# Kernel tuning notes

Measured on AMD Instinct MI355X. Metric: run time of the kernel, lower is better.

## Reference

```python
import jax, jax.numpy as jnp
import numpy as np

N_HEADS = 16


def layernorm(x, g, b, eps=1e-5):
    mu = jnp.mean(x, axis=-1, keepdims=True)
    var = jnp.var(x, axis=-1, keepdims=True)
    return (x - mu) * jax.lax.rsqrt(var + eps) * g + b


def mha(x, w_qkv, b_qkv, w_o, b_o, n_heads):
    # standard multi-head self-attention (dropout off / eval mode)
    B, S, D = x.shape
    hd = D // n_heads
    qkv = x @ w_qkv + b_qkv                      # [B,S,3D]
    q, k, v = jnp.split(qkv, 3, axis=-1)
    q = q.reshape(B, S, n_heads, hd).transpose(0, 2, 1, 3)  # bhsd
    k = k.reshape(B, S, n_heads, hd).transpose(0, 2, 1, 3)
    v = v.reshape(B, S, n_heads, hd).transpose(0, 2, 1, 3)
    att = jnp.einsum('bhqd,bhkd->bhqk', q, k) / jnp.sqrt(jnp.asarray(hd, x.dtype))
    att = jax.nn.softmax(att, axis=-1)
    out = jnp.einsum('bhqk,bhkd->bhqd', att, v)
    out = out.transpose(0, 2, 1, 3).reshape(B, S, D)
    return out @ w_o + b_o


def setup_inputs() -> dict:
    key = jax.random.key(0)
    ks = jax.random.split(key, 12)
    B, Sx, Sz, D = 4, 1024, 1024, 1024
    H = D * 4
    s = 0.02
    return {
        'x': jax.random.normal(ks[0], (B, Sx, D), jnp.float32),
        'z': jax.random.normal(ks[1], (B, Sz, D), jnp.float32),
        'g1': jnp.ones((D,), jnp.float32),
        'b1': jnp.zeros((D,), jnp.float32),
        'w_qkv': jax.random.normal(ks[2], (D, 3 * D), jnp.float32) * s,
        'b_qkv': jnp.zeros((3 * D,), jnp.float32),
        'w_o': jax.random.normal(ks[3], (D, D), jnp.float32) * s,
        'b_o': jnp.zeros((D,), jnp.float32),
        'w_kv': jax.random.normal(ks[4], (D, 2 * D), jnp.float32) * s,
        'b_kv': jnp.zeros((2 * D,), jnp.float32),
        'g2': jnp.ones((D,), jnp.float32),
        'b2': jnp.zeros((D,), jnp.float32),
        'w_m1': jax.random.normal(ks[5], (D, H), jnp.float32) * s,
        'b_m1': jnp.zeros((H,), jnp.float32),
        'w_m2': jax.random.normal(ks[6], (H, D), jnp.float32) * s,
        'b_m2': jnp.zeros((D,), jnp.float32),
    }


def reference(x, z, g1, b1, w_qkv, b_qkv, w_o, b_o, w_kv, b_kv, g2, b2, w_m1, b_m1, w_m2, b_m2):
    # q = x + self_mha(ln1(x))
    q = x + mha(layernorm(x, g1, b1), w_qkv, b_qkv, w_o, b_o, N_HEADS)
    # single-head cross attention: k,v from z, scale by sqrt(dim)
    kv = z @ w_kv + b_kv
    k, v = jnp.split(kv, 2, axis=-1)            # each [B,Sz,D]
    scale = jnp.sqrt(jnp.asarray(k.shape[-1], x.dtype))
    att = jax.nn.softmax(jnp.einsum('bqd,bkd->bqk', q, k) / scale, axis=-1)
    out = jnp.einsum('bqk,bkd->bqd', att, v)
    # out = out + mlp(ln2(out))
    h = layernorm(out, g2, b2)
    h = jax.nn.gelu(h @ w_m1 + b_m1) @ w_m2 + b_m2
    return out + h
```

## Files before the change

### kernel.cpp

```cpp
#include <hip/hip_runtime.h>
#include <cstdint>
#include <cstddef>

using u16 = unsigned short;

typedef __attribute__((ext_vector_type(4))) float f32x4;
typedef __attribute__((ext_vector_type(8))) short bf16x8;

#define DEV static __device__ __forceinline__

DEV float bf2f(u16 v) {
  union { unsigned u; float f; } x; x.u = ((unsigned)v) << 16; return x.f;
}
DEV u16 f2bf(float f) {
  union { float f; unsigned u; } x; x.f = f;
  unsigned r = x.u + 0x7fffu + ((x.u >> 16) & 1u);
  return (u16)(r >> 16);
}
DEV void gload16(const void* g, void* l) {
  __builtin_amdgcn_global_load_lds((const __attribute__((address_space(1))) void*)g,
                                   (__attribute__((address_space(3))) void*)l, 16, 0, 0);
}
DEV float fast_gelu(float x) {
  float y = 0.7978845608028654f * (x + 0.044715f * x * x * x);
  y = fminf(fmaxf(y, -15.0f), 15.0f);
  float e = __expf(2.0f * y);
  float t = (e - 1.0f) / (e + 1.0f);
  return 0.5f * x * (1.0f + t);
}

DEV float rowmax16_dpp(float v) {
  union { float f; int i; } a, b;
  a.f = v;
  b.i = __builtin_amdgcn_update_dpp(0, a.i, 0x121, 0xf, 0xf, true); a.f = fmaxf(a.f, b.f);
  b.i = __builtin_amdgcn_update_dpp(0, a.i, 0x122, 0xf, 0xf, true); a.f = fmaxf(a.f, b.f);
  b.i = __builtin_amdgcn_update_dpp(0, a.i, 0x124, 0xf, 0xf, true); a.f = fmaxf(a.f, b.f);
  b.i = __builtin_amdgcn_update_dpp(0, a.i, 0x128, 0xf, 0xf, true); a.f = fmaxf(a.f, b.f);
  return a.f;
}

template <typename OutT, bool GELU, int BN, bool SPLIT>
__global__ __launch_bounds__(256, 2) void gemm_nt(
    const u16* __restrict__ A, const u16* __restrict__ Bt, OutT* __restrict__ C,
    int K, int lda, int ldb, int ldc,
    const float* __restrict__ bias,
    const float* __restrict__ resF, const u16* __restrict__ resB, int ldr,
    float scale,
    long long sA, long long sB, long long sC, long long sR,
    int kSlices)
{
  constexpr int NW = (BN == 128) ? 64 : 32;
  constexpr int NJ = NW / 16;
  __shared__ u16 As[128 * 32];
  __shared__ u16 Bs[BN * 32];

  const int z = blockIdx.z;
  const int bz = z / kSlices;
  const int ks = z - bz * kSlices;
  const int Ksl = K / kSlices;
  const int kbeg = ks * Ksl, kend = kbeg + Ksl;

  A  += (size_t)bz * sA;
  Bt += (size_t)bz * sB;
  if constexpr (SPLIT) C += (size_t)ks * sC;
  else                 C += (size_t)bz * sC;
  const int m0 = blockIdx.y * 128, n0 = blockIdx.x * BN;
  const int tid = threadIdx.x;
  const int lane = tid & 63, wave = tid >> 6;
  const int wm = (wave >> 1) * 64, wn = (wave & 1) * NW;
  const int m15 = lane & 15, quad = lane >> 4;

  const u16* Ab = A + (size_t)m0 * lda;
  const u16* Bb = Bt + (size_t)n0 * ldb;
  const int r0 = tid >> 2, cc8 = (tid & 3) * 8;

  f32x4 acc[4][NJ];
#pragma unroll
  for (int i = 0; i < 4; i++)
#pragma unroll
    for (int j = 0; j < NJ; j++) acc[i][j] = (f32x4){0.f, 0.f, 0.f, 0.f};

  for (int k0 = kbeg; k0 < kend; k0 += 32) {
    __syncthreads();
    gload16(Ab + (size_t)r0 * lda + k0 + cc8,        &As[tid * 8]);
    gload16(Ab + (size_t)(r0 + 64) * lda + k0 + cc8, &As[2048 + tid * 8]);
    gload16(Bb + (size_t)r0 * ldb + k0 + cc8,        &Bs[tid * 8]);
    if constexpr (BN == 128)
      gload16(Bb + (size_t)(r0 + 64) * ldb + k0 + cc8, &Bs[2048 + tid * 8]);
    __syncthreads();
    bf16x8 af[4], bfr[NJ];
#pragma unroll
    for (int i = 0; i < 4; i++) af[i]  = *(const bf16x8*)&As[(wm + i * 16 + m15) * 32 + quad * 8];
#pragma unroll
    for (int j = 0; j < NJ; j++) bfr[j] = *(const bf16x8*)&Bs[(wn + j * 16 + m15) * 32 + quad * 8];
#pragma unroll
    for (int i = 0; i < 4; i++)
#pragma unroll
      for (int j = 0; j < NJ; j++)
        acc[i][j] = __builtin_amdgcn_mfma_f32_16x16x32_bf16(af[i], bfr[j], acc[i][j], 0, 0, 0);
  }

  const float* resFb = resF ? resF + (size_t)bz * sR : nullptr;
  const u16*   resBb = resB ? resB + (size_t)bz * sR : nullptr;

#pragma unroll
  for (int i = 0; i < 4; i++) {
    const int rowb = m0 + wm + i * 16 + quad * 4;
#pragma unroll
    for (int r = 0; r < 4; r++) {
      const size_t rowoff = (size_t)(rowb + r) * ldc;
      const size_t resoff = (size_t)(rowb + r) * ldr;
#pragma unroll
      for (int j = 0; j < NJ; j++) {
        const int col = n0 + wn + j * 16 + m15;
        float v = acc[i][j][r] * scale;
        if constexpr (SPLIT) {
          ((u16*)C)[rowoff + col] = f2bf(v);
        } else {
          if (bias) v += bias[col];
          if (GELU) v = fast_gelu(v);
          if (resFb) v += resFb[resoff + col];
          if (resBb) v += bf2f(resBb[resoff + col]);
          if constexpr (sizeof(OutT) == 4) C[rowoff + col] = v;
          else ((u16*)C)[rowoff + col] = f2bf(v);
        }
      }
    }
  }
}

__global__ __launch_bounds__(256) void mlp2_reduce_k(
    const u16* __restrict__ part, long long sliceStride,
    const u16* __restrict__ outb, const float* __restrict__ b_m2,
    float* __restrict__ outF)
{
  const size_t i = (size_t)blockIdx.x * 256 + threadIdx.x;
  const int col = (int)((i * 4) & 1023);
  const ushort4 u = ((const ushort4*)outb)[i];
  float4 o;
  o.x = bf2f(u.x) + b_m2[col + 0];
  o.y = bf2f(u.y) + b_m2[col + 1];
  o.z = bf2f(u.z) + b_m2[col + 2];
  o.w = bf2f(u.w) + b_m2[col + 3];
#pragma unroll
  for (int ks = 0; ks < 4; ks++) {
    const ushort4 p = ((const ushort4*)(part + (size_t)ks * sliceStride))[i];
    o.x += bf2f(p.x); o.y += bf2f(p.y); o.z += bf2f(p.z); o.w += bf2f(p.w);
  }
  ((float4*)outF)[i] = o;
}

__global__ __launch_bounds__(256) void transpose_all_k(
    const float* __restrict__ w_qkv, const float* __restrict__ w_o,
    const float* __restrict__ w_kv,  const float* __restrict__ w_m1,
    const float* __restrict__ w_m2,
    u16* __restrict__ wqkvT, u16* __restrict__ woT, u16* __restrict__ wkvT,
    u16* __restrict__ wm1T,  u16* __restrict__ wm2T)
{
  __shared__ u16 tile[32][33];
  int idx = blockIdx.x;
  const float* in; u16* out; int gx, ldin, ldout;
  if (idx < 3072)      { in = w_qkv; out = wqkvT; gx = 96;  ldin = 3072; ldout = 1024; }
  else if (idx < 4096) { idx -= 3072; in = w_o;  out = woT;  gx = 32;  ldin = 1024; ldout = 1024; }
  else if (idx < 6144) { idx -= 4096; in = w_kv; out = wkvT; gx = 64;  ldin = 2048; ldout = 1024; }
  else if (idx < 10240){ idx -= 6144; in = w_m1; out = wm1T; gx = 128; ldin = 4096; ldout = 1024; }
  else                 { idx -= 10240; in = w_m2; out = wm2T; gx = 32; ldin = 1024; ldout = 4096; }
  const int bx = idx % gx, by = idx / gx;
  const int tx = threadIdx.x & 31, ty = threadIdx.x >> 5;
  const int x = bx * 32 + tx;
#pragma unroll
  for (int j = 0; j < 4; j++)
    tile[ty + j * 8][tx] = f2bf(in[(size_t)(by * 32 + ty + j * 8) * ldin + x]);
  __syncthreads();
  const int x2 = by * 32 + tx;
#pragma unroll
  for (int j = 0; j < 4; j++)
    out[(size_t)(bx * 32 + ty + j * 8) * ldout + x2] = tile[tx][ty + j * 8];
}

__global__ __launch_bounds__(256) void transpose_v_self(
    const u16* __restrict__ qkv, u16* __restrict__ vT)
{
  __shared__ u16 tile[32][33];
  const int z = blockIdx.z, b = z >> 4, h = z & 15;
  const u16* in = qkv + (size_t)b * 1024 * 3072 + 2048 + h * 64;
  u16* out = vT + (size_t)z * 64 * 1024;
  const int tx = threadIdx.x & 31, ty = threadIdx.x >> 5;
  const int key0 = blockIdx.x * 32, d0 = blockIdx.y * 32;
#pragma unroll
  for (int j = 0; j < 4; j++)
    tile[ty + j * 8][tx] = in[(size_t)(key0 + ty + j * 8) * 3072 + d0 + tx];
  __syncthreads();
#pragma unroll
  for (int j = 0; j < 4; j++)
    out[(size_t)(d0 + ty + j * 8) * 1024 + key0 + tx] = tile[tx][ty + j * 8];
}

__global__ __launch_bounds__(256, 5) void flash_self_attn3(
    const u16* __restrict__ qkv, const u16* __restrict__ vT, u16* __restrict__ outp)
{
  __shared__ u16 Ks[64 * 72];
  __shared__ u16 Vs[64 * 72];
  __shared__ u16 Ps[4][16 * 72];
  const int b = blockIdx.z, h = blockIdx.y, q0 = blockIdx.x * 64;
  const int tid = threadIdx.x;
  const int lane = tid & 63, w = tid >> 6;
  const int m15 = lane & 15, quad = lane >> 4;
  const float L2E = 1.4426950408889634f;

  const size_t base = (size_t)b * 1024 * 3072;
  const u16* qb  = qkv + base + (size_t)q0 * 3072 + h * 64;
  const u16* kb  = qkv + base + 1024 + h * 64;
  const u16* vtb = vT + (size_t)(b * 16 + h) * 64 * 1024;

  const int r8 = tid >> 3, c8 = (tid & 7) * 8;

  bf16x8 aq[2];
#pragma unroll
  for (int kk = 0; kk < 2; kk++) {
    const bf16x8 raw = *(const bf16x8*)(qb + (size_t)(w * 16 + m15) * 3072 + kk * 32 + quad * 8);
#pragma unroll
    for (int j = 0; j < 8; j++)
      ((u16*)&aq[kk])[j] = f2bf(bf2f(((const u16*)&raw)[j]) * 0.125f);
  }

  const short oneb = (short)0x3F80;
  const bf16x8 ones = {oneb, oneb, oneb, oneb, oneb, oneb, oneb, oneb};

  float mL[4];
  f32x4 lacc;
  f32x4 oacc[4];
#pragma unroll
  for (int r = 0; r < 4; r++) mL[r] = -3.0e38f;
  lacc = (f32x4){0.f, 0.f, 0.f, 0.f};
#pragma unroll
  for (int d = 0; d < 4; d++) oacc[d] = (f32x4){0.f, 0.f, 0.f, 0.f};

  for (int kt = 0; kt < 16; kt++) {
    const int key0 = kt * 64;
    bf16x8 kreg[2], vreg[2];
#pragma unroll
    for (int i = 0; i < 2; i++) {
      kreg[i] = *(const bf16x8*)(kb + (size_t)(key0 + r8 + i * 32) * 3072 + c8);
      vreg[i] = *(const bf16x8*)(vtb + (size_t)(r8 + i * 32) * 1024 + key0 + c8);
    }
    __syncthreads();
#pragma unroll
    for (int i = 0; i < 2; i++) {
      *(bf16x8*)&Ks[(r8 + i * 32) * 72 + c8] = kreg[i];
      *(bf16x8*)&Vs[(r8 + i * 32) * 72 + c8] = vreg[i];
    }
    __syncthreads();

    f32x4 sacc[4];
#pragma unroll
    for (int n = 0; n < 4; n++) sacc[n] = (f32x4){0.f, 0.f, 0.f, 0.f};
#pragma unroll
    for (int kk = 0; kk < 2; kk++)
#pragma unroll
      for (int n = 0; n < 4; n++) {
        const bf16x8 bk = *(const bf16x8*)&Ks[(n * 16 + m15) * 72 + kk * 32 + quad * 8];
        sacc[n] = __builtin_amdgcn_mfma_f32_16x16x32_bf16(aq[kk], bk, sacc[n], 0, 0, 0);
      }

    float al[4];
#pragma unroll
    for (int r = 0; r < 4; r++) {
      float v = fmaxf(fmaxf(sacc[0][r], sacc[1][r]), fmaxf(sacc[2][r], sacc[3][r]));
      v = rowmax16_dpp(v) * L2E;
      const float mnew = fmaxf(mL[r], v);
      al[r] = __builtin_amdgcn_exp2f(mL[r] - mnew);
      mL[r] = mnew;
    }
#pragma unroll
    for (int n = 0; n < 4; n++)
#pragma unroll
      for (int r = 0; r < 4; r++) {
        const float p = __builtin_amdgcn_exp2f(fmaf(sacc[n][r], L2E, -mL[r]));
        Ps[w][(quad * 4 + r) * 72 + n * 16 + m15] = f2bf(p);
      }
#pragma unroll
    for (int r = 0; r < 4; r++) {
      lacc[r] *= al[r];
#pragma unroll
      for (int d = 0; d < 4; d++) oacc[d][r] *= al[r];
    }

    bf16x8 ap[2];
    ap[0] = *(const bf16x8*)&Ps[w][m15 * 72 + quad * 8];
    ap[1] = *(const bf16x8*)&Ps[w][m15 * 72 + 32 + quad * 8];
    lacc = __builtin_amdgcn_mfma_f32_16x16x32_bf16(ap[0], ones, lacc, 0, 0, 0);
    lacc = __builtin_amdgcn_mfma_f32_16x16x32_bf16(ap[1], ones, lacc, 0, 0, 0);
#pragma unroll
    for (int kk = 0; kk < 2; kk++)
#pragma unroll
      for (int d = 0; d < 4; d++) {
        const bf16x8 bv = *(const bf16x8*)&Vs[(d * 16 + m15) * 72 + kk * 32 + quad * 8];
        oacc[d] = __builtin_amdgcn_mfma_f32_16x16x32_bf16(ap[kk], bv, oacc[d], 0, 0, 0);
      }
  }

  u16* ob = outp + (size_t)(b * 1024 + q0 + w * 16 + quad * 4) * 1024 + h * 64 + m15;
#pragma unroll
  for (int r = 0; r < 4; r++) {
    const float inv = 1.0f / lacc[r];
#pragma unroll
    for (int d = 0; d < 4; d++)
      ob[(size_t)r * 1024 + d * 16] = f2bf(oacc[d][r] * inv);
  }
}

template <typename TIn>
__global__ __launch_bounds__(256) void layernorm_k(
    const TIn* __restrict__ x, const float* __restrict__ g, const float* __restrict__ bb,
    u16* __restrict__ y)
{
  const int row = blockIdx.x;
  const int t = threadIdx.x;
  float v[4];
  if constexpr (sizeof(TIn) == 4) {
    const float4 f = ((const float4*)((const float*)x + (size_t)row * 1024))[t];
    v[0] = f.x; v[1] = f.y; v[2] = f.z; v[3] = f.w;
  } else {
    const ushort4 u = ((const ushort4*)((const u16*)x + (size_t)row * 1024))[t];
    v[0] = bf2f(u.x); v[1] = bf2f(u.y); v[2] = bf2f(u.z); v[3] = bf2f(u.w);
  }
  float s = v[0] + v[1] + v[2] + v[3];
  float sq = v[0]*v[0] + v[1]*v[1] + v[2]*v[2] + v[3]*v[3];
#pragma unroll
  for (int off = 1; off < 64; off <<= 1) { s += __shfl_xor(s, off); sq += __shfl_xor(sq, off); }
  __shared__ float red[8];
  const int wv = t >> 6;
  if ((t & 63) == 0) { red[wv] = s; red[4 + wv] = sq; }
  __syncthreads();
  s = red[0] + red[1] + red[2] + red[3];
  sq = red[4] + red[5] + red[6] + red[7];
  const float mean = s * (1.0f / 1024.0f);
  const float var = sq * (1.0f / 1024.0f) - mean * mean;
  const float rstd = rsqrtf(var + 1e-5f);
  const int c = t * 4;
  ushort4 o;
  o.x = f2bf((v[0] - mean) * rstd * g[c + 0] + bb[c + 0]);
  o.y = f2bf((v[1] - mean) * rstd * g[c + 1] + bb[c + 1]);
  o.z = f2bf((v[2] - mean) * rstd * g[c + 2] + bb[c + 2]);
  o.w = f2bf((v[3] - mean) * rstd * g[c + 3] + bb[c + 3]);
  ((ushort4*)(y + (size_t)row * 1024))[t] = o;
}

__global__ __launch_bounds__(256) void softmax_rows_k(const float* __restrict__ S, u16* __restrict__ P)
{
  const int row = blockIdx.x;
  const int t = threadIdx.x;
  const float4 f = ((const float4*)(S + (size_t)row * 1024))[t];
  float mx = fmaxf(fmaxf(f.x, f.y), fmaxf(f.z, f.w));
#pragma unroll
  for (int off = 1; off < 64; off <<= 1) mx = fmaxf(mx, __shfl_xor(mx, off));
  __shared__ float red[8];
  const int wv = t >> 6;
  if ((t & 63) == 0) red[wv] = mx;
  __syncthreads();
  mx = fmaxf(fmaxf(red[0], red[1]), fmaxf(red[2], red[3]));
  float e0 = __expf(f.x - mx), e1 = __expf(f.y - mx), e2 = __expf(f.z - mx), e3 = __expf(f.w - mx);
  float s = e0 + e1 + e2 + e3;
#pragma unroll
  for (int off = 1; off < 64; off <<= 1) s += __shfl_xor(s, off);
  if ((t & 63) == 0) red[4 + wv] = s;
  __syncthreads();
  s = red[4] + red[5] + red[6] + red[7];
  const float inv = 1.0f / s;
  ushort4 o; o.x = f2bf(e0 * inv); o.y = f2bf(e1 * inv); o.z = f2bf(e2 * inv); o.w = f2bf(e3 * inv);
  ((ushort4*)(P + (size_t)row * 1024))[t] = o;
}

__global__ __launch_bounds__(256) void transpose_k(
    const u16* __restrict__ in, u16* __restrict__ out,
    int ldin, int ldout, long long sIn, long long sOut)
{
  __shared__ u16 tile[32][33];
  in  += (size_t)blockIdx.z * sIn;
  out += (size_t)blockIdx.z * sOut;
  const int tx = threadIdx.x & 31, ty = threadIdx.x >> 5;
  const int x = blockIdx.x * 32 + tx;
#pragma unroll
  for (int j = 0; j < 4; j++)
    tile[ty + j * 8][tx] = in[(size_t)(blockIdx.y * 32 + ty + j * 8) * ldin + x];
  __syncthreads();
  const int x2 = blockIdx.y * 32 + tx;
#pragma unroll
  for (int j = 0; j < 4; j++)
    out[(size_t)(blockIdx.x * 32 + ty + j * 8) * ldout + x2] = tile[tx][ty + j * 8];
}

__global__ __launch_bounds__(256) void cast_f2b_k(const float* __restrict__ in, u16* __restrict__ out)
{
  const size_t i = (size_t)blockIdx.x * 256 + threadIdx.x;
  const float4 f = ((const float4*)in)[i];
  ushort4 o; o.x = f2bf(f.x); o.y = f2bf(f.y); o.z = f2bf(f.z); o.w = f2bf(f.w);
  ((ushort4*)out)[i] = o;
}

extern "C" void kernel_launch(void* const* d_in, const int* in_sizes, int n_in,
                              void* d_out, int out_size, void* d_ws, size_t ws_size,
                              hipStream_t stream)
{
  const float* x     = (const float*)d_in[0];
  const float* z     = (const float*)d_in[1];
  const float* g1    = (const float*)d_in[2];
  const float* b1    = (const float*)d_in[3];
  const float* w_qkv = (const float*)d_in[4];
  const float* b_qkv = (const float*)d_in[5];
  const float* w_o   = (const float*)d_in[6];
  const float* b_o   = (const float*)d_in[7];
  const float* w_kv  = (const float*)d_in[8];
  const float* b_kv  = (const float*)d_in[9];
  const float* g2    = (const float*)d_in[10];
  const float* b2    = (const float*)d_in[11];
  const float* w_m1  = (const float*)d_in[12];
  const float* b_m1  = (const float*)d_in[13];
  const float* w_m2  = (const float*)d_in[14];
  const float* b_m2  = (const float*)d_in[15];
  float* outF = (float*)d_out;

  char* ws = (char*)d_ws;
  const size_t MB = 1024ull * 1024ull;
  u16*   qkv   = (u16*)(ws + 0);
  u16*   Pm    = (u16*)(ws + 0);
  u16*   hm    = (u16*)(ws + 0);
  u16*   zb    = (u16*)(ws + 24 * MB);
  u16*   vTs   = (u16*)(ws + 24 * MB);
  u16*   xln   = (u16*)(ws + 32 * MB);
  u16*   mpart = (u16*)(ws + 32 * MB);
  u16*   qbuf  = (u16*)(ws + 40 * MB);
  u16*   kv    = (u16*)(ws + 48 * MB);
  float* Ssc   = (float*)(ws + 64 * MB);
  u16*   h1    = (u16*)(ws + 64 * MB);
  u16*   outb  = (u16*)(ws + 80 * MB);
  u16*   wqkvT = (u16*)(ws + 88 * MB);
  u16*   woT   = (u16*)(ws + 94 * MB);
  u16*   wkvT  = (u16*)(ws + 96 * MB);
  u16*   wm1T  = (u16*)(ws + 100 * MB);
  u16*   wm2T  = (u16*)(ws + 108 * MB);
  u16*   vT    = (u16*)(ws + 116 * MB);

  dim3 blk(256);
  const long long M1 = 1024 * 1024;

  hipLaunchKernelGGL(transpose_all_k, dim3(14336), blk, 0, stream,
                     w_qkv, w_o, w_kv, w_m1, w_m2, wqkvT, woT, wkvT, wm1T, wm2T);

  hipLaunchKernelGGL(cast_f2b_k, dim3(4096), blk, 0, stream, z, zb);
  hipLaunchKernelGGL((layernorm_k<float>), dim3(4096), blk, 0, stream, x, g1, b1, xln);

  hipLaunchKernelGGL((gemm_nt<u16, false, 128, false>), dim3(16, 32, 1), blk, 0, stream,
                     zb, wkvT, kv, 1024, 1024, 1024, 2048,
                     b_kv, (const float*)nullptr, (const u16*)nullptr, 0, 1.0f, 0LL, 0LL, 0LL, 0LL, 1);
  hipLaunchKernelGGL((gemm_nt<u16, false, 128, false>), dim3(24, 32, 1), blk, 0, stream,
                     xln, wqkvT, qkv, 1024, 1024, 1024, 3072,
                     b_qkv, (const float*)nullptr, (const u16*)nullptr, 0, 1.0f, 0LL, 0LL, 0LL, 0LL, 1);
  hipLaunchKernelGGL(transpose_v_self, dim3(32, 2, 64), blk, 0, stream, qkv, vTs);
  hipLaunchKernelGGL(flash_self_attn3, dim3(16, 16, 4), blk, 0, stream, qkv, vTs, xln);
  hipLaunchKernelGGL((gemm_nt<u16, false, 64, false>), dim3(16, 32, 1), blk, 0, stream,
                     xln, woT, qbuf, 1024, 1024, 1024, 1024,
                     b_o, x, (const u16*)nullptr, 1024, 1.0f, 0LL, 0LL, 0LL, 0LL, 1);
  hipLaunchKernelGGL((gemm_nt<float, false, 64, false>), dim3(16, 8, 4), blk, 0, stream,
                     qbuf, kv, Ssc, 1024, 1024, 2048, 1024,
                     (const float*)nullptr, (const float*)nullptr, (const u16*)nullptr, 0,
                     0.03125f, M1, 2 * M1, M1, 0LL, 1);
  hipLaunchKernelGGL(softmax_rows_k, dim3(4096), blk, 0, stream, Ssc, Pm);
  hipLaunchKernelGGL(transpose_k, dim3(32, 32, 4), blk, 0, stream,
                     kv + 1024, vT, 2048, 1024, 2 * M1, M1);
  hipLaunchKernelGGL((gemm_nt<u16, false, 64, false>), dim3(16, 8, 4), blk, 0, stream,
                     Pm, vT, outb, 1024, 1024, 1024, 1024,
                     (const float*)nullptr, (const float*)nullptr, (const u16*)nullptr, 0,
                     1.0f, M1, M1, M1, 0LL, 1);
  hipLaunchKernelGGL((layernorm_k<u16>), dim3(4096), blk, 0, stream, (const u16*)outb, g2, b2, h1);
  hipLaunchKernelGGL((gemm_nt<u16, true, 128, false>), dim3(32, 32, 1), blk, 0, stream,
                     h1, wm1T, hm, 1024, 1024, 1024, 4096,
                     b_m1, (const float*)nullptr, (const u16*)nullptr, 0, 1.0f, 0LL, 0LL, 0LL, 0LL, 1);
  hipLaunchKernelGGL((gemm_nt<u16, false, 128, true>), dim3(8, 32, 4), blk, 0, stream,
                     hm, wm2T, mpart, 4096, 4096, 4096, 1024,
                     (const float*)nullptr, (const float*)nullptr, (const u16*)nullptr, 0,
                     1.0f, 0LL, 0LL, 4LL * M1, 0LL, 4);
  hipLaunchKernelGGL(mlp2_reduce_k, dim3(4096), blk, 0, stream,
                     mpart, 4LL * M1, outb, b_m2, outF);
}
```

Baseline: 499.8 us.

## Fuse z cast with first layernorm, cheapen GELU, raise GEMM occupancy hint

Merges the z float-to-bf16 cast and the x layernorm into one two-slice launch, which removes a kernel launch. It also rewrites GELU's tanh using the hardware exp2 and reciprocal intrinsics without clamping, and raises the GEMM launch_bounds minimum blocks per CU from 2 to 4. The higher occupancy hint may force register spilling in the MFMA GEMM. The unclamped exp2 can overflow to inf for large inputs, but the reciprocal then yields t=1, so the result stays correct.

```diff
diff --git a/kernel.cpp b/kernel.cpp
--- a/kernel.cpp
+++ b/kernel.cpp
@@ -22,10 +22,9 @@
                                    (__attribute__((address_space(3))) void*)l, 16, 0, 0);
 }
 DEV float fast_gelu(float x) {
-  float y = 0.7978845608028654f * (x + 0.044715f * x * x * x);
-  y = fminf(fmaxf(y, -15.0f), 15.0f);
-  float e = __expf(2.0f * y);
-  float t = (e - 1.0f) / (e + 1.0f);
+  const float y = 0.7978845608028654f * (x + 0.044715f * x * x * x);
+  const float e = __builtin_amdgcn_exp2f(y * 2.8853900817779268f);
+  const float t = 1.0f - 2.0f * __builtin_amdgcn_rcpf(e + 1.0f);
   return 0.5f * x * (1.0f + t);
 }
 
@@ -40,7 +39,7 @@
 }
 
 template <typename OutT, bool GELU, int BN, bool SPLIT>
-__global__ __launch_bounds__(256, 2) void gemm_nt(
+__global__ __launch_bounds__(256, 4) void gemm_nt(
     const u16* __restrict__ A, const u16* __restrict__ Bt, OutT* __restrict__ C,
     int K, int lda, int ldb, int ldc,
     const float* __restrict__ bias,
@@ -178,6 +177,44 @@
     out[(size_t)(bx * 32 + ty + j * 8) * ldout + x2] = tile[tx][ty + j * 8];
 }
 
+__global__ __launch_bounds__(256) void prep_k(
+    const float* __restrict__ x, const float* __restrict__ g, const float* __restrict__ bb,
+    u16* __restrict__ xln, const float* __restrict__ z, u16* __restrict__ zb)
+{
+  const int row = blockIdx.x;
+  const int t = threadIdx.x;
+  if (blockIdx.y == 1) {
+    const size_t i = (size_t)row * 256 + t;
+    const float4 f = ((const float4*)z)[i];
+    ushort4 o; o.x = f2bf(f.x); o.y = f2bf(f.y); o.z = f2bf(f.z); o.w = f2bf(f.w);
+    ((ushort4*)zb)[i] = o;
+    return;
+  }
+  float v[4];
+  const float4 f = ((const float4*)(x + (size_t)row * 1024))[t];
+  v[0] = f.x; v[1] = f.y; v[2] = f.z; v[3] = f.w;
+  float s = v[0] + v[1] + v[2] + v[3];
+  float sq = v[0]*v[0] + v[1]*v[1] + v[2]*v[2] + v[3]*v[3];
+#pragma unroll
+  for (int off = 1; off < 64; off <<= 1) { s += __shfl_xor(s, off); sq += __shfl_xor(sq, off); }
+  __shared__ float red[8];
+  const int wv = t >> 6;
+  if ((t & 63) == 0) { red[wv] = s; red[4 + wv] = sq; }
+  __syncthreads();
+  s = red[0] + red[1] + red[2] + red[3];
+  sq = red[4] + red[5] + red[6] + red[7];
+  const float mean = s * (1.0f / 1024.0f);
+  const float var = sq * (1.0f / 1024.0f) - mean * mean;
+  const float rstd = rsqrtf(var + 1e-5f);
+  const int c = t * 4;
+  ushort4 o;
+  o.x = f2bf((v[0] - mean) * rstd * g[c + 0] + bb[c + 0]);
+  o.y = f2bf((v[1] - mean) * rstd * g[c + 1] + bb[c + 1]);
+  o.z = f2bf((v[2] - mean) * rstd * g[c + 2] + bb[c + 2]);
+  o.w = f2bf((v[3] - mean) * rstd * g[c + 3] + bb[c + 3]);
+  ((ushort4*)(xln + (size_t)row * 1024))[t] = o;
+}
+
 __global__ __launch_bounds__(256) void transpose_v_self(
     const u16* __restrict__ qkv, u16* __restrict__ vT)
 {
@@ -310,21 +347,15 @@
   }
 }
 
-template <typename TIn>
-__global__ __launch_bounds__(256) void layernorm_k(
-    const TIn* __restrict__ x, const float* __restrict__ g, const float* __restrict__ bb,
+__global__ __launch_bounds__(256) void layernorm_b_k(
+    const u16* __restrict__ x, const float* __restrict__ g, const float* __restrict__ bb,
     u16* __restrict__ y)
 {
   const int row = blockIdx.x;
   const int t = threadIdx.x;
   float v[4];
-  if constexpr (sizeof(TIn) == 4) {
-    const float4 f = ((const float4*)((const float*)x + (size_t)row * 1024))[t];
-    v[0] = f.x; v[1] = f.y; v[2] = f.z; v[3] = f.w;
-  } else {
-    const ushort4 u = ((const ushort4*)((const u16*)x + (size_t)row * 1024))[t];
-    v[0] = bf2f(u.x); v[1] = bf2f(u.y); v[2] = bf2f(u.z); v[3] = bf2f(u.w);
-  }
+  const ushort4 u = ((const ushort4*)(x + (size_t)row * 1024))[t];
+  v[0] = bf2f(u.x); v[1] = bf2f(u.y); v[2] = bf2f(u.z); v[3] = bf2f(u.w);
   float s = v[0] + v[1] + v[2] + v[3];
   float sq = v[0]*v[0] + v[1]*v[1] + v[2]*v[2] + v[3]*v[3];
 #pragma unroll
@@ -389,14 +420,6 @@
 #pragma unroll
   for (int j = 0; j < 4; j++)
     out[(size_t)(blockIdx.x * 32 + ty + j * 8) * ldout + x2] = tile[tx][ty + j * 8];
-}
-
-__global__ __launch_bounds__(256) void cast_f2b_k(const float* __restrict__ in, u16* __restrict__ out)
-{
-  const size_t i = (size_t)blockIdx.x * 256 + threadIdx.x;
-  const float4 f = ((const float4*)in)[i];
-  ushort4 o; o.x = f2bf(f.x); o.y = f2bf(f.y); o.z = f2bf(f.z); o.w = f2bf(f.w);
-  ((ushort4*)out)[i] = o;
 }
 
 extern "C" void kernel_launch(void* const* d_in, const int* in_sizes, int n_in,
@@ -447,9 +470,7 @@
 
   hipLaunchKernelGGL(transpose_all_k, dim3(14336), blk, 0, stream,
                      w_qkv, w_o, w_kv, w_m1, w_m2, wqkvT, woT, wkvT, wm1T, wm2T);
-
-  hipLaunchKernelGGL(cast_f2b_k, dim3(4096), blk, 0, stream, z, zb);
-  hipLaunchKernelGGL((layernorm_k<float>), dim3(4096), blk, 0, stream, x, g1, b1, xln);
+  hipLaunchKernelGGL(prep_k, dim3(4096, 2), blk, 0, stream, x, g1, b1, xln, z, zb);
 
   hipLaunchKernelGGL((gemm_nt<u16, false, 128, false>), dim3(16, 32, 1), blk, 0, stream,
                      zb, wkvT, kv, 1024, 1024, 1024, 2048,
@@ -473,7 +494,7 @@
                      Pm, vT, outb, 1024, 1024, 1024, 1024,
                      (const float*)nullptr, (const float*)nullptr, (const u16*)nullptr, 0,
                      1.0f, M1, M1, M1, 0LL, 1);
-  hipLaunchKernelGGL((layernorm_k<u16>), dim3(4096), blk, 0, stream, (const u16*)outb, g2, b2, h1);
+  hipLaunchKernelGGL(layernorm_b_k, dim3(4096), blk, 0, stream, (const u16*)outb, g2, b2, h1);
   hipLaunchKernelGGL((gemm_nt<u16, true, 128, false>), dim3(32, 32, 1), blk, 0, stream,
                      h1, wm1T, hm, 1024, 1024, 1024, 4096,
                      b_m1, (const float*)nullptr, (const u16*)nullptr, 0, 1.0f, 0LL, 0LL, 0LL, 0LL, 1);
```

Measured after the change: 502.6 us. Within noise of the previous version (+0.5%).
